# Kernel optimization log

Hardware: AMD Instinct MI355X
Metric: run time of the kernel (lower is better)

## Reference

```python
import jax, jax.numpy as jnp
import numpy as np

L, H, B = 16, 1024, 4096


def setup_inputs() -> dict:
    key = jax.random.key(0)
    k1, k2, k3, k4 = jax.random.split(key, 4)
    z = jax.random.normal(k1, (B, H), dtype=jnp.float32)
    layer_ids = jax.random.randint(k2, (B,), 0, L)
    # Module initializes weight = identity per layer; add small noise so the
    # transform is non-trivial while staying near the module's init regime.
    eye = jnp.broadcast_to(jnp.eye(H, dtype=jnp.float32), (L, H, H))
    weight = eye + 0.02 * jax.random.normal(k3, (L, H, H), dtype=jnp.float32)
    bias = 0.02 * jax.random.normal(k4, (L, H), dtype=jnp.float32)
    return {"z": z, "layer_ids": layer_ids, "weight": weight, "bias": bias}


def reference(z, layer_ids, weight, bias):
    # Faithful math: out[b] = weight[layer_ids[b]] @ z[b] + bias[layer_ids[b]].
    # Instead of materializing the gathered [B,H,H] weight tensor (as torch.bmm
    # forces), compute all-layer outputs with a grouped GEMM [B,L,H] and select.
    out_all = jnp.einsum('lij,bj->bli', weight, z)  # [B, L, H]
    out = jnp.take_along_axis(out_all, layer_ids[:, None, None], axis=1)[:, 0, :]  # [B, H]
    return out + bias[layer_ids]
```

## Files before the change

### kernel.cpp

```cpp
#include <hip/hip_runtime.h>


#define HDIM 1024
#define LNUM 16
#define BTOT 4096

constexpr int BM = 64, BN = 128, BK = 32;
constexpr int NT = HDIM / BK;
constexpr int MSLOTS = 8;

constexpr int AROW = 128;
constexpr int BROW = 80;
constexpr int AOFF = 0;
constexpr int BOFF = 8192;
constexpr int BUFSZ = 8192 + 128 * 80;

typedef __attribute__((ext_vector_type(4))) float floatx4;
typedef __attribute__((ext_vector_type(2))) __fp16 cvt16x2;
typedef __attribute__((ext_vector_type(8))) _Float16 f16x8;
typedef __attribute__((ext_vector_type(2))) unsigned int uintx2;

#define LDS_BARRIER()                                          \
    do {                                                       \
        asm volatile("s_waitcnt lgkmcnt(0)" ::: "memory");     \
        __builtin_amdgcn_s_barrier();                          \
    } while (0)

__device__ __forceinline__ void split4(floatx4 v, uintx2& hw, uintx2& lw) {
    cvt16x2 h01 = __builtin_amdgcn_cvt_pkrtz(v[0], v[1]);
    cvt16x2 h23 = __builtin_amdgcn_cvt_pkrtz(v[2], v[3]);
    cvt16x2 l01 = __builtin_amdgcn_cvt_pkrtz(v[0] - (float)h01[0],
                                             v[1] - (float)h01[1]);
    cvt16x2 l23 = __builtin_amdgcn_cvt_pkrtz(v[2] - (float)h23[0],
                                             v[3] - (float)h23[1]);
    hw[0] = __builtin_bit_cast(unsigned int, h01);
    hw[1] = __builtin_bit_cast(unsigned int, h23);
    lw[0] = __builtin_bit_cast(unsigned int, l01);
    lw[1] = __builtin_bit_cast(unsigned int, l23);
}

__device__ __forceinline__ uintx2 cvt4_rtn(floatx4 v) {
    _Float16 h0 = (_Float16)v[0], h1 = (_Float16)v[1];
    _Float16 h2 = (_Float16)v[2], h3 = (_Float16)v[3];
    uintx2 r;
    r[0] = (unsigned)__builtin_bit_cast(unsigned short, h0)
         | ((unsigned)__builtin_bit_cast(unsigned short, h1) << 16);
    r[1] = (unsigned)__builtin_bit_cast(unsigned short, h2)
         | ((unsigned)__builtin_bit_cast(unsigned short, h3) << 16);
    return r;
}

__global__ __launch_bounds__(256, 3) void fused_grouped_mfma_kernel(
    const float* __restrict__ z,
    const int* __restrict__ layer_ids,
    const float* __restrict__ weight,
    const float* __restrict__ bias,
    float* __restrict__ out) {

    const int bid  = blockIdx.x;
    const int xcd  = bid & 7;
    const int slot = bid >> 3;
    const int l    = xcd + ((slot >> 6) << 3);
    const int rem  = slot & 63;
    const int my   = rem >> 3;
    const int nx   = rem & 7;
    const int n0   = nx * BN;

    const int tid  = threadIdx.x;
    const int lane = tid & 63;
    const int w    = tid >> 6;
    const int wm   = w & 1;
    const int wn   = w >> 1;

    __shared__ __align__(16) unsigned char sm[2][BUFSZ];
    __shared__ int permTile[BM];
    __shared__ int waveSums[4];

    const int4* lid4 = (const int4*)layer_ids;
    unsigned mask = 0;
#pragma unroll
    for (int q = 0; q < 4; ++q) {
        int4 v = lid4[tid * 4 + q];
        mask |= (unsigned)(v.x == l) << (4 * q)
             |  (unsigned)(v.y == l) << (4 * q + 1)
             |  (unsigned)(v.z == l) << (4 * q + 2)
             |  (unsigned)(v.w == l) << (4 * q + 3);
    }
    const int ct = __popc(mask);
    int x = ct;
#pragma unroll
    for (int o = 1; o < 64; o <<= 1) {
        int v = __shfl_up(x, o);
        if (lane >= o) x += v;
    }
    if (lane == 63) waveSums[w] = x;
    __syncthreads();
    int waveBase = 0, cnt = 0;
#pragma unroll
    for (int w2 = 0; w2 < 4; ++w2) {
        int s = waveSums[w2];
        if (w2 < w) waveBase += s;
        cnt += s;
    }
    const int et = waveBase + x - ct;

    const int kq  = tid & 7;
    const int rb  = tid >> 3;
    const int swz = (rb & 7) << 1;
    const int wA_hi = AOFF + rb * AROW + ((kq ^ swz) << 3);
    const int wA_lo = AOFF + rb * AROW + (((8 + kq) ^ swz) << 3);
    const int wB    = BOFF + rb * BROW + (kq << 3);

    const int lr = lane & 15;
    const int ks = lane >> 4;
    const int rdA_hi = AOFF + (wm * 32 + lr) * AROW + ((ks ^ (lr & 7)) << 4);
    const int rdA_lo = AOFF + (wm * 32 + lr) * AROW + (((4 + ks) ^ (lr & 7)) << 4);
    const int rdB    = BOFF + (wn * 64 + lr) * BROW + (ks << 4);

    const float* wBase = weight + (size_t)l * HDIM * HDIM;
    const int colBase = n0 + wn * 64 + lr;
    float bb[4];
#pragma unroll
    for (int j = 0; j < 4; ++j) bb[j] = bias[l * HDIM + colBase + j * 16];

    for (int m0 = my * BM; m0 < cnt; m0 += MSLOTS * BM) {
        __syncthreads();
        {
            unsigned m2 = mask;
            int r = et;
            while (m2) {
                int p = __ffs(m2) - 1;
                m2 &= m2 - 1;
                unsigned rr = (unsigned)(r - m0);
                if (rr < (unsigned)BM) permTile[rr] = tid * 16 + p;
                ++r;
            }
        }
        __syncthreads();

        const float* aPtr[2];
        const float* bPtr[4];
#pragma unroll
        for (int p = 0; p < 2; ++p) {
            int gm = rb + 32 * p;
            if (gm > cnt - 1 - m0) gm = cnt - 1 - m0;
            aPtr[p] = z + (size_t)permTile[gm] * HDIM + kq * 4;
        }
#pragma unroll
        for (int p = 0; p < 4; ++p)
            bPtr[p] = wBase + (size_t)(n0 + rb + 32 * p) * HDIM + kq * 4;

        floatx4 acc[2][4] = {};
        floatx4 av[2], bv[4];

        auto loadT = [&](int k0) {
#pragma unroll
            for (int p = 0; p < 2; ++p) av[p] = *(const floatx4*)(aPtr[p] + k0);
#pragma unroll
            for (int p = 0; p < 4; ++p) bv[p] = *(const floatx4*)(bPtr[p] + k0);
        };

        auto stageT = [&](unsigned char* buf) {
            uintx2 hw, lw;
#pragma unroll
            for (int p = 0; p < 2; ++p) {
                split4(av[p], hw, lw);
                *(uintx2*)(buf + wA_hi + p * 32 * AROW) = hw;
                *(uintx2*)(buf + wA_lo + p * 32 * AROW) = lw;
            }
#pragma unroll
            for (int p = 0; p < 4; ++p)
                *(uintx2*)(buf + wB + p * 32 * BROW) = cvt4_rtn(bv[p]);
        };

        auto compute = [&](const unsigned char* buf) {
            f16x8 ah[2], al[2], bh[4];
#pragma unroll
            for (int i = 0; i < 2; ++i) {
                ah[i] = *(const f16x8*)(buf + rdA_hi + i * 16 * AROW);
                al[i] = *(const f16x8*)(buf + rdA_lo + i * 16 * AROW);
            }
#pragma unroll
            for (int j = 0; j < 4; ++j)
                bh[j] = *(const f16x8*)(buf + rdB + j * 16 * BROW);
#pragma unroll
            for (int i = 0; i < 2; ++i)
#pragma unroll
                for (int j = 0; j < 4; ++j) {
                    acc[i][j] = __builtin_amdgcn_mfma_f32_16x16x32_f16(
                        ah[i], bh[j], acc[i][j], 0, 0, 0);
                    acc[i][j] = __builtin_amdgcn_mfma_f32_16x16x32_f16(
                        al[i], bh[j], acc[i][j], 0, 0, 0);
                }
        };

        loadT(0);
        stageT(sm[0]);
        loadT(BK);
        LDS_BARRIER();

#pragma unroll 1
        for (int t2 = 0; t2 < NT; t2 += 2) {
            stageT(sm[1]);
            if (t2 + 2 < NT) loadT((t2 + 2) * BK);
            compute(sm[0]);
            LDS_BARRIER();

            if (t2 + 2 < NT) stageT(sm[0]);
            if (t2 + 3 < NT) loadT((t2 + 3) * BK);
            compute(sm[1]);
            LDS_BARRIER();
        }

        const int rq = lane >> 4;
#pragma unroll
        for (int i = 0; i < 2; ++i) {
#pragma unroll
            for (int v = 0; v < 4; ++v) {
                int gm = wm * 32 + i * 16 + rq * 4 + v;
                if (m0 + gm < cnt) {
                    float* o = out + (size_t)permTile[gm] * HDIM + colBase;
#pragma unroll
                    for (int j = 0; j < 4; ++j) o[j * 16] = acc[i][j][v] + bb[j];
                }
            }
        }
    }
}

extern "C" void kernel_launch(void* const* d_in, const int* in_sizes, int n_in,
                              void* d_out, int out_size, void* d_ws, size_t ws_size,
                              hipStream_t stream) {
    const float* z = nullptr;
    const int* layer_ids = nullptr;
    const float* weight = nullptr;
    const float* bias = nullptr;
    for (int i = 0; i < n_in; ++i) {
        switch (in_sizes[i]) {
            case BTOT * HDIM:        z = (const float*)d_in[i]; break;
            case BTOT:               layer_ids = (const int*)d_in[i]; break;
            case LNUM * HDIM * HDIM: weight = (const float*)d_in[i]; break;
            case LNUM * HDIM:        bias = (const float*)d_in[i]; break;
        }
    }
    float* out = (float*)d_out;

    fused_grouped_mfma_kernel<<<dim3(1024), 256, 0, stream>>>(
        z, layer_ids, weight, bias, out);
}
```

Before: 136.3 us.

## Double the K tile to 64 with wider 16-byte LDS staging and relaid swizzle

Raises BK from 32 to 64, which halves the number of K iterations and barriers. Each thread now loads two float4s per row and writes 16-byte fp16 hi/lo words to LDS with a new XOR swizzle. The MFMA loop is reordered to issue all hi-part products before the lo-part products within each 32-wide K slice. This doubles LDS per block and lowers launch bounds occupancy from 3 to 2 blocks, and the extra registers held per load may reduce latency hiding.

```diff
diff --git a/kernel.cpp b/kernel.cpp
--- a/kernel.cpp
+++ b/kernel.cpp
@@ -5,20 +5,20 @@
 #define LNUM 16
 #define BTOT 4096
 
-constexpr int BM = 64, BN = 128, BK = 32;
+constexpr int BM = 64, BN = 128, BK = 64;
 constexpr int NT = HDIM / BK;
 constexpr int MSLOTS = 8;
 
-constexpr int AROW = 128;
-constexpr int BROW = 80;
+constexpr int AROW = 256;
+constexpr int BROW = 144;
 constexpr int AOFF = 0;
-constexpr int BOFF = 8192;
-constexpr int BUFSZ = 8192 + 128 * 80;
+constexpr int BOFF = 16384;
+constexpr int BUFSZ = 16384 + 128 * 144;
 
 typedef __attribute__((ext_vector_type(4))) float floatx4;
 typedef __attribute__((ext_vector_type(2))) __fp16 cvt16x2;
 typedef __attribute__((ext_vector_type(8))) _Float16 f16x8;
-typedef __attribute__((ext_vector_type(2))) unsigned int uintx2;
+typedef __attribute__((ext_vector_type(4))) unsigned int uintx4;
 
 #define LDS_BARRIER()                                          \
     do {                                                       \
@@ -26,31 +26,44 @@
         __builtin_amdgcn_s_barrier();                          \
     } while (0)
 
-__device__ __forceinline__ void split4(floatx4 v, uintx2& hw, uintx2& lw) {
-    cvt16x2 h01 = __builtin_amdgcn_cvt_pkrtz(v[0], v[1]);
-    cvt16x2 h23 = __builtin_amdgcn_cvt_pkrtz(v[2], v[3]);
-    cvt16x2 l01 = __builtin_amdgcn_cvt_pkrtz(v[0] - (float)h01[0],
-                                             v[1] - (float)h01[1]);
-    cvt16x2 l23 = __builtin_amdgcn_cvt_pkrtz(v[2] - (float)h23[0],
-                                             v[3] - (float)h23[1]);
+__device__ __forceinline__ void split8(floatx4 v0, floatx4 v1,
+                                       uintx4& hw, uintx4& lw) {
+    cvt16x2 h01 = __builtin_amdgcn_cvt_pkrtz(v0[0], v0[1]);
+    cvt16x2 h23 = __builtin_amdgcn_cvt_pkrtz(v0[2], v0[3]);
+    cvt16x2 h45 = __builtin_amdgcn_cvt_pkrtz(v1[0], v1[1]);
+    cvt16x2 h67 = __builtin_amdgcn_cvt_pkrtz(v1[2], v1[3]);
+    cvt16x2 l01 = __builtin_amdgcn_cvt_pkrtz(v0[0] - (float)h01[0],
+                                             v0[1] - (float)h01[1]);
+    cvt16x2 l23 = __builtin_amdgcn_cvt_pkrtz(v0[2] - (float)h23[0],
+                                             v0[3] - (float)h23[1]);
+    cvt16x2 l45 = __builtin_amdgcn_cvt_pkrtz(v1[0] - (float)h45[0],
+                                             v1[1] - (float)h45[1]);
+    cvt16x2 l67 = __builtin_amdgcn_cvt_pkrtz(v1[2] - (float)h67[0],
+                                             v1[3] - (float)h67[1]);
     hw[0] = __builtin_bit_cast(unsigned int, h01);
     hw[1] = __builtin_bit_cast(unsigned int, h23);
+    hw[2] = __builtin_bit_cast(unsigned int, h45);
+    hw[3] = __builtin_bit_cast(unsigned int, h67);
     lw[0] = __builtin_bit_cast(unsigned int, l01);
     lw[1] = __builtin_bit_cast(unsigned int, l23);
-}
-
-__device__ __forceinline__ uintx2 cvt4_rtn(floatx4 v) {
-    _Float16 h0 = (_Float16)v[0], h1 = (_Float16)v[1];
-    _Float16 h2 = (_Float16)v[2], h3 = (_Float16)v[3];
-    uintx2 r;
-    r[0] = (unsigned)__builtin_bit_cast(unsigned short, h0)
-         | ((unsigned)__builtin_bit_cast(unsigned short, h1) << 16);
-    r[1] = (unsigned)__builtin_bit_cast(unsigned short, h2)
-         | ((unsigned)__builtin_bit_cast(unsigned short, h3) << 16);
+    lw[2] = __builtin_bit_cast(unsigned int, l45);
+    lw[3] = __builtin_bit_cast(unsigned int, l67);
+}
+
+__device__ __forceinline__ uintx4 cvt8_rtn(floatx4 v0, floatx4 v1) {
+    uintx4 r;
+    r[0] = (unsigned)__builtin_bit_cast(unsigned short, (_Float16)v0[0])
+         | ((unsigned)__builtin_bit_cast(unsigned short, (_Float16)v0[1]) << 16);
+    r[1] = (unsigned)__builtin_bit_cast(unsigned short, (_Float16)v0[2])
+         | ((unsigned)__builtin_bit_cast(unsigned short, (_Float16)v0[3]) << 16);
+    r[2] = (unsigned)__builtin_bit_cast(unsigned short, (_Float16)v1[0])
+         | ((unsigned)__builtin_bit_cast(unsigned short, (_Float16)v1[1]) << 16);
+    r[3] = (unsigned)__builtin_bit_cast(unsigned short, (_Float16)v1[2])
+         | ((unsigned)__builtin_bit_cast(unsigned short, (_Float16)v1[3]) << 16);
     return r;
 }
 
-__global__ __launch_bounds__(256, 3) void fused_grouped_mfma_kernel(
+__global__ __launch_bounds__(256, 2) void fused_grouped_mfma_kernel(
     const float* __restrict__ z,
     const int* __restrict__ layer_ids,
     const float* __restrict__ weight,
@@ -104,17 +117,17 @@
     }
     const int et = waveBase + x - ct;
 
-    const int kq  = tid & 7;
+    const int kc  = tid & 7;
     const int rb  = tid >> 3;
-    const int swz = (rb & 7) << 1;
-    const int wA_hi = AOFF + rb * AROW + ((kq ^ swz) << 3);
-    const int wA_lo = AOFF + rb * AROW + (((8 + kq) ^ swz) << 3);
-    const int wB    = BOFF + rb * BROW + (kq << 3);
+    const int aswz = rb & 7;
+    const int wA_hi = AOFF + rb * AROW + ((kc ^ aswz) << 4);
+    const int wA_lo = wA_hi + 128;
+    const int wB    = BOFF + rb * BROW + (kc << 4);
 
     const int lr = lane & 15;
     const int ks = lane >> 4;
     const int rdA_hi = AOFF + (wm * 32 + lr) * AROW + ((ks ^ (lr & 7)) << 4);
-    const int rdA_lo = AOFF + (wm * 32 + lr) * AROW + (((4 + ks) ^ (lr & 7)) << 4);
+    const int rdA_lo = rdA_hi + 128;
     const int rdB    = BOFF + (wn * 64 + lr) * BROW + (ks << 4);
 
     const float* wBase = weight + (size_t)l * HDIM * HDIM;
@@ -144,54 +157,68 @@
         for (int p = 0; p < 2; ++p) {
             int gm = rb + 32 * p;
             if (gm > cnt - 1 - m0) gm = cnt - 1 - m0;
-            aPtr[p] = z + (size_t)permTile[gm] * HDIM + kq * 4;
+            aPtr[p] = z + (size_t)permTile[gm] * HDIM + kc * 8;
         }
 #pragma unroll
         for (int p = 0; p < 4; ++p)
-            bPtr[p] = wBase + (size_t)(n0 + rb + 32 * p) * HDIM + kq * 4;
+            bPtr[p] = wBase + (size_t)(n0 + rb + 32 * p) * HDIM + kc * 8;
 
         floatx4 acc[2][4] = {};
-        floatx4 av[2], bv[4];
+        floatx4 av[2][2], bv[4][2];
 
         auto loadT = [&](int k0) {
 #pragma unroll
-            for (int p = 0; p < 2; ++p) av[p] = *(const floatx4*)(aPtr[p] + k0);
-#pragma unroll
-            for (int p = 0; p < 4; ++p) bv[p] = *(const floatx4*)(bPtr[p] + k0);
+            for (int p = 0; p < 2; ++p) {
+                av[p][0] = *(const floatx4*)(aPtr[p] + k0);
+                av[p][1] = *(const floatx4*)(aPtr[p] + k0 + 4);
+            }
+#pragma unroll
+            for (int p = 0; p < 4; ++p) {
+                bv[p][0] = *(const floatx4*)(bPtr[p] + k0);
+                bv[p][1] = *(const floatx4*)(bPtr[p] + k0 + 4);
+            }
         };
 
         auto stageT = [&](unsigned char* buf) {
-            uintx2 hw, lw;
+            uintx4 hw, lw;
 #pragma unroll
             for (int p = 0; p < 2; ++p) {
-                split4(av[p], hw, lw);
-                *(uintx2*)(buf + wA_hi + p * 32 * AROW) = hw;
-                *(uintx2*)(buf + wA_lo + p * 32 * AROW) = lw;
+                split8(av[p][0], av[p][1], hw, lw);
+                *(uintx4*)(buf + wA_hi + p * 32 * AROW) = hw;
+                *(uintx4*)(buf + wA_lo + p * 32 * AROW) = lw;
             }
 #pragma unroll
             for (int p = 0; p < 4; ++p)
-                *(uintx2*)(buf + wB + p * 32 * BROW) = cvt4_rtn(bv[p]);
+                *(uintx4*)(buf + wB + p * 32 * BROW) = cvt8_rtn(bv[p][0], bv[p][1]);
         };
 
         auto compute = [&](const unsigned char* buf) {
-            f16x8 ah[2], al[2], bh[4];
-#pragma unroll
-            for (int i = 0; i < 2; ++i) {
-                ah[i] = *(const f16x8*)(buf + rdA_hi + i * 16 * AROW);
-                al[i] = *(const f16x8*)(buf + rdA_lo + i * 16 * AROW);
-            }
-#pragma unroll
-            for (int j = 0; j < 4; ++j)
-                bh[j] = *(const f16x8*)(buf + rdB + j * 16 * BROW);
-#pragma unroll
-            for (int i = 0; i < 2; ++i)
-#pragma unroll
-                for (int j = 0; j < 4; ++j) {
-                    acc[i][j] = __builtin_amdgcn_mfma_f32_16x16x32_f16(
-                        ah[i], bh[j], acc[i][j], 0, 0, 0);
-                    acc[i][j] = __builtin_amdgcn_mfma_f32_16x16x32_f16(
-                        al[i], bh[j], acc[i][j], 0, 0, 0);
+#pragma unroll
+            for (int kk = 0; kk < 2; ++kk) {
+                const int axor = kk * 64;
+                const int boff = kk * 64;
+                f16x8 ah[2], al[2], bh[4];
+#pragma unroll
+                for (int i = 0; i < 2; ++i) {
+                    ah[i] = *(const f16x8*)(buf + ((rdA_hi + i * 16 * AROW) ^ axor));
+                    al[i] = *(const f16x8*)(buf + ((rdA_lo + i * 16 * AROW) ^ axor));
                 }
+#pragma unroll
+                for (int j = 0; j < 4; ++j)
+                    bh[j] = *(const f16x8*)(buf + rdB + j * 16 * BROW + boff);
+#pragma unroll
+                for (int i = 0; i < 2; ++i)
+#pragma unroll
+                    for (int j = 0; j < 4; ++j)
+                        acc[i][j] = __builtin_amdgcn_mfma_f32_16x16x32_f16(
+                            ah[i], bh[j], acc[i][j], 0, 0, 0);
+#pragma unroll
+                for (int i = 0; i < 2; ++i)
+#pragma unroll
+                    for (int j = 0; j < 4; ++j)
+                        acc[i][j] = __builtin_amdgcn_mfma_f32_16x16x32_f16(
+                            al[i], bh[j], acc[i][j], 0, 0, 0);
+            }
         };
 
         loadT(0);
```

Result: slower. 142.8 us (+4.8%).
